# Kernel tuning notes

Measured on AMD Instinct MI355X. Metric: run time of the kernel, lower is better.

Reference implementation:

```python
import math
import jax, jax.numpy as jnp
import numpy as np

B, T, C, H = 4, 2048, 1024, 16
HS = C // H


def setup_inputs() -> dict:
    key = jax.random.key(0)
    ks = jax.random.split(key, 5)
    s_in = 1.0 / math.sqrt(C)
    return {
        "x": jax.random.normal(ks[0], (B, T, C), dtype=jnp.float32),
        "w_attn": jax.random.normal(ks[1], (C, 3 * C), dtype=jnp.float32) * s_in,
        "b_attn": jax.random.normal(ks[2], (3 * C,), dtype=jnp.float32) * 0.02,
        "w_proj": jax.random.normal(ks[3], (C, C), dtype=jnp.float32) * s_in,
        "b_proj": jax.random.normal(ks[4], (C,), dtype=jnp.float32) * 0.02,
    }


def reference(x, w_attn, b_attn, w_proj, b_proj):
    Bx, Tx, Cx = x.shape
    hs = Cx // H
    qkv = x @ w_attn + b_attn  # [B, T, 3C]
    q, k, v = jnp.split(qkv, 3, axis=-1)
    # [B, H, T, hs]
    q = q.reshape(Bx, Tx, H, hs).transpose(0, 2, 1, 3)
    k = k.reshape(Bx, Tx, H, hs).transpose(0, 2, 1, 3)
    v = v.reshape(Bx, Tx, H, hs).transpose(0, 2, 1, 3)
    scale = 1.0 / math.sqrt(hs)
    att = jnp.einsum("bhqd,bhkd->bhqk", q, k) * scale  # [B, H, T, T]
    causal = jnp.tril(jnp.ones((Tx, Tx), dtype=bool))
    att = jnp.where(causal, att, -jnp.inf)
    att = jax.nn.softmax(att, axis=-1)
    y = jnp.einsum("bhqk,bhkd->bhqd", att, v)  # [B, H, T, hs]
    y = y.transpose(0, 2, 1, 3).reshape(Bx, Tx, Cx)
    return y @ w_proj + b_proj
```

## Files before the change

kernel.cpp:

```cpp
#include <hip/hip_runtime.h>
#include <stdint.h>

#define Bn 4
#define Tn 2048
#define Cn 1024
#define Hn 16
#define HSn 64
#define Mn (Bn*Tn)
#define N1n (3*Cn)

typedef unsigned short u16;
typedef unsigned int u32;
typedef __attribute__((ext_vector_type(8))) short short8;
typedef __attribute__((ext_vector_type(4))) float f32x4;
typedef __attribute__((ext_vector_type(16))) float f32x16;

#define QSCf (0.125f * 1.44269504f)

__device__ __forceinline__ u16 f2bf(float f){
  u32 u = __float_as_uint(f);
  u += 0x7fffu + ((u >> 16) & 1u);
  return (u16)(u >> 16);
}

__device__ __forceinline__ u32 pkbf(float lo, float hi_){
  u32 r; asm("v_cvt_pk_bf16_f32 %0, %1, %2" : "=v"(r) : "v"(lo), "v"(hi_)); return r;
}

__device__ __forceinline__ float fexp2(float x){
  float r; asm("v_exp_f32 %0, %1" : "=v"(r) : "v"(x)); return r;
}

__device__ __forceinline__ float fmax3(float a, float b, float c){
  float r; asm("v_max3_f32 %0, %1, %2, %3" : "=v"(r) : "v"(a), "v"(b), "v"(c)); return r;
}

__device__ __forceinline__ void plswap(u32 &a, u32 &b){
  auto r = __builtin_amdgcn_permlane32_swap(a, b, false, false);
  a = r[0]; b = r[1];
}

__device__ __forceinline__ void gload_lds16(const void* g, void* l){
  __builtin_amdgcn_global_load_lds(
      (const __attribute__((address_space(1))) u32*)g,
      (__attribute__((address_space(3))) u32*)l, 16, 0, 0);
}

#define BARRIER() __builtin_amdgcn_s_barrier()
#define CFENCE() asm volatile("" ::: "memory")

__device__ __forceinline__ void tcvt_body(const float* __restrict__ in,
                                          u16* __restrict__ out,
                                          int R, int Cc, int bxx, int byy,
                                          float sh[64][68]){
  int tid = threadIdx.x;
  int c0 = bxx*64, r0 = byy*64;
  int rr = tid >> 4, c4 = (tid & 15) * 4;
  #pragma unroll
  for (int p=0;p<4;p++){
    int r = rr + 16*p;
    *(float4*)&sh[r][c4] = *(const float4*)&in[(size_t)(r0+r)*Cc + c0 + c4];
  }
  __syncthreads();
  #pragma unroll
  for (int p=0;p<4;p++){
    int oc = rr + 16*p;
    u32 w0 = (u32)f2bf(sh[c4+0][oc]) | ((u32)f2bf(sh[c4+1][oc]) << 16);
    u32 w1 = (u32)f2bf(sh[c4+2][oc]) | ((u32)f2bf(sh[c4+3][oc]) << 16);
    uint2 pk; pk.x = w0; pk.y = w1;
    *(uint2*)&out[(size_t)(c0+oc)*R + r0 + c4] = pk;
  }
}

__global__ __launch_bounds__(256)
void k_pre(const float* __restrict__ x, const float* __restrict__ wa,
           const float* __restrict__ wp, u16* __restrict__ xb,
           u16* __restrict__ waT, u16* __restrict__ wpT){
  __shared__ float sh[64][68];
  int bid = blockIdx.x;
  if (bid < 4096){
    int i = bid*256 + threadIdx.x;
    const float4* p = (const float4*)(x) + (size_t)i*2;
    float4 a = p[0], b = p[1];
    uint4 r;
    r.x = (u32)f2bf(a.x) | ((u32)f2bf(a.y) << 16);
    r.y = (u32)f2bf(a.z) | ((u32)f2bf(a.w) << 16);
    r.z = (u32)f2bf(b.x) | ((u32)f2bf(b.y) << 16);
    r.w = (u32)f2bf(b.z) | ((u32)f2bf(b.w) << 16);
    *((uint4*)(xb) + i) = r;
  } else if (bid < 4096 + 768){
    int b2 = bid - 4096;
    tcvt_body(wa, waT, Cn, N1n, b2 % 48, b2 / 48, sh);
  } else {
    int b3 = bid - 4864;
    tcvt_body(wp, wpT, Cn, Cn, b3 % 16, b3 / 16, sh);
  }
}

template <int MODE>
__global__ __launch_bounds__(256, 2)
void k_gemm2(const u16* __restrict__ A, const u16* __restrict__ Bt,
             const float* __restrict__ bias, void* __restrict__ Cout,
             u16* __restrict__ vt, int Nn_, int byPerXcd)
{
  extern __shared__ char smem[];
  const int nkt = 16;
  int tid = threadIdx.x;
  int wave = tid >> 6, lane = tid & 63, g = lane >> 4, cl = lane & 15;
  int wm = wave >> 1, wn = wave & 1;

  int xcd = blockIdx.x & 7, idx = blockIdx.x >> 3;
  int by = xcd * byPerXcd + (idx % byPerXcd);
  int bx = idx / byPerXcd;
  int m0 = by * 128, n0 = bx * 128;

  int srow = tid >> 3;
  int scolb = (tid & 7) << 4;
  int ssw = scolb ^ ((srow & 7) << 4);
  const char* Agp = (const char*)A  + (size_t)(m0 + srow) * 2048 + ssw;
  const char* Bgp = (const char*)Bt + (size_t)(n0 + srow) * 2048 + ssw;

  #define STG(t_, b_) { \
    const char* ag = Agp + (size_t)(t_)*128; \
    const char* bg = Bgp + (size_t)(t_)*128; \
    char* ab = smem + (b_)*32768 + (wave<<10); \
    char* bb = ab + 16384; \
    gload_lds16(ag,          ab); \
    gload_lds16(ag+ 65536,   ab+4096); \
    gload_lds16(ag+131072,   ab+8192); \
    gload_lds16(ag+196608,   ab+12288); \
    gload_lds16(bg,          bb); \
    gload_lds16(bg+ 65536,   bb+4096); \
    gload_lds16(bg+131072,   bb+8192); \
    gload_lds16(bg+196608,   bb+12288); }

  f32x4 acc[4][4];
  #pragma unroll
  for (int i=0;i<4;i++)
    #pragma unroll
    for (int j=0;j<4;j++) acc[i][j] = (f32x4){0.f,0.f,0.f,0.f};

  STG(0, 0);

  for (int t=0; t<nkt; ++t){
    int b = t & 1;
    if (t+1 < nkt){
      STG(t+1, b^1);
      asm volatile("s_waitcnt vmcnt(8)" ::: "memory");
    } else {
      asm volatile("s_waitcnt vmcnt(0)" ::: "memory");
    }
    BARRIER(); CFENCE();
    const char* Asb = smem + b*32768;
    const char* Bsb = Asb + 16384;
    short8 a[4][2], bq[4][2];
    #pragma unroll
    for (int i=0;i<4;i++){
      int row = wm*64 + i*16 + cl;
      #pragma unroll
      for (int ks=0;ks<2;ks++)
        a[i][ks] = *(const short8*)(Asb + row*128 + ((ks*64 + g*16) ^ ((row&7)<<4)));
    }
    #pragma unroll
    for (int j=0;j<4;j++){
      int row = wn*64 + j*16 + cl;
      #pragma unroll
      for (int ks=0;ks<2;ks++)
        bq[j][ks] = *(const short8*)(Bsb + row*128 + ((ks*64 + g*16) ^ ((row&7)<<4)));
    }
    __builtin_amdgcn_s_setprio(1);
    #pragma unroll
    for (int ks=0;ks<2;ks++)
      #pragma unroll
      for (int i=0;i<4;i++)
        #pragma unroll
        for (int j=0;j<4;j++)
          acc[i][j] = __builtin_amdgcn_mfma_f32_16x16x32_bf16(a[i][ks], bq[j][ks], acc[i][j], 0, 0, 0);
    __builtin_amdgcn_s_setprio(0);
    CFENCE(); BARRIER(); CFENCE();
  }
  #undef STG

  #pragma unroll
  for (int jj=0;jj<4;jj++){
    int col = n0 + wn*64 + jj*16 + cl;
    float bj = bias[col];
    if (MODE == 0){
      #pragma unroll
      for (int i=0;i<4;i++){
        int rowb = m0 + wm*64 + i*16 + g*4;
        #pragma unroll
        for (int r=0;r<4;r++)
          ((float*)Cout)[(size_t)(rowb+r)*Nn_ + col] = acc[i][jj][r] + bj;
      }
    } else if (col < 2*Cn){
      float sc = (col < Cn) ? QSCf : 1.0f;
      #pragma unroll
      for (int i=0;i<4;i++){
        int rowb = m0 + wm*64 + i*16 + g*4;
        #pragma unroll
        for (int r=0;r<4;r++)
          ((u16*)Cout)[(size_t)(rowb+r)*Nn_ + col] = f2bf((acc[i][jj][r] + bj) * sc);
      }
    } else {
      int hd = col - 2*Cn;
      #pragma unroll
      for (int i=0;i<4;i++){
        int rowb = m0 + wm*64 + i*16 + g*4;
        int bb = rowb >> 11, tt = rowb & 2047;
        u16* dst = vt + (((size_t)(bb*16 + (hd>>6)))*64 + (hd&63))*2048 + tt;
        uint2 pk;
        pk.x = (u32)f2bf(acc[i][jj][0]+bj) | ((u32)f2bf(acc[i][jj][1]+bj) << 16);
        pk.y = (u32)f2bf(acc[i][jj][2]+bj) | ((u32)f2bf(acc[i][jj][3]+bj) << 16);
        *(uint2*)dst = pk;
      }
    }
  }
}

__global__ __launch_bounds__(256, 4)
void k_attn(const u16* __restrict__ qkv, const u16* __restrict__ vt, u16* __restrict__ yb){
  __shared__ __align__(16) u16 Ks[2][64*64];
  __shared__ __align__(16) u16 Vs[2][64*64];
  int tid = threadIdx.x, wave = tid >> 6, lane = tid & 63;
  int ql = lane & 31, hi = lane >> 5;
  int blk = blockIdx.x;
  int xcd = blk & 7, rest = blk >> 3;
  int bh  = xcd + 8*(rest & 7);
  int qtsel = rest >> 3;
  int a_ = qtsel & 3, g_ = qtsel >> 2;
  int qt = (g_==0) ? (15 - a_) : (g_==1) ? (7 - a_) : (g_==2) ? (8 + a_) : a_;
  int b = bh >> 4, h = bh & 15;

  const u16* Kbase = qkv + (size_t)b*Tn*N1n + Cn + h*HSn;
  const u16* Vbase = vt  + (size_t)bh*HSn*Tn;

  auto STAGE = [&](int bufi, int kt){
    int kb_ = kt*64;
    #pragma unroll
    for (int it=0; it<2; ++it){
      int off = it*4096 + tid*16;
      int row = off >> 7;
      int cb  = off & 127;
      int gc  = (cb ^ ((row & 7) << 4)) >> 1;
      gload_lds16(Kbase + (size_t)(kb_ + row)*N1n + gc,
                  (char*)&Ks[bufi][0] + it*4096 + (wave << 10));
      gload_lds16(Vbase + (size_t)row*Tn + kb_ + gc,
                  (char*)&Vs[bufi][0] + it*4096 + (wave << 10));
    }
  };

  int q0 = qt * 128;
  int qw0 = q0 + wave*32;
  int qg  = qw0 + ql;
  int ntiles = 2*qt + 2;

  const u16* Qp = qkv + (size_t)(b*Tn + qg)*N1n + h*HSn;
  short8 qf[4];
  #pragma unroll
  for (int dc=0; dc<4; ++dc) qf[dc] = *(const short8*)&Qp[dc*16 + hi*8];

  short8 ones;
  #pragma unroll
  for (int r=0; r<8; ++r) ones[r] = (short)0x3F80;

  f32x16 accO[2], accL;
  #pragma unroll
  for (int f=0; f<2; ++f)
    #pragma unroll
    for (int r=0; r<16; ++r) accO[f][r] = 0.f;
  #pragma unroll
  for (int r=0; r<16; ++r) accL[r] = 0.f;
  float m_ = -1e30f;

  int xsw = (ql & 7) << 4;

  auto PVS = [&](const f32x16& sx, int pb, int voff, const char* Vsb){
    u32 w0 = pkbf(sx[pb+0], sx[pb+1]);
    u32 w1 = pkbf(sx[pb+2], sx[pb+3]);
    u32 w2 = pkbf(sx[pb+4], sx[pb+5]);
    u32 w3 = pkbf(sx[pb+6], sx[pb+7]);
    plswap(w0, w2);
    plswap(w1, w3);
    union { u32 w[4]; short8 v; } pu;
    pu.w[0] = w0; pu.w[1] = w1; pu.w[2] = w2; pu.w[3] = w3;
    __builtin_amdgcn_s_setprio(1);
    #pragma unroll
    for (int f=0; f<2; ++f){
      short8 vf = *(const short8*)(Vsb + ((f*32 + ql) << 7) + ((voff + hi*16) ^ xsw));
      accO[f] = __builtin_amdgcn_mfma_f32_32x32x16_bf16(vf, pu.v, accO[f], 0, 0, 0);
    }
    accL = __builtin_amdgcn_mfma_f32_32x32x16_bf16(ones, pu.v, accL, 0, 0, 0);
    __builtin_amdgcn_s_setprio(0);
  };

  STAGE(0, 0);
  int buf = 0;

  for (int kt=0; kt<ntiles; ++kt){
    if (kt+1 < ntiles){
      STAGE(buf^1, kt+1);
      asm volatile("s_waitcnt vmcnt(4)" ::: "memory");
    } else {
      asm volatile("s_waitcnt vmcnt(0)" ::: "memory");
    }
    BARRIER(); CFENCE();
    const char* Ksb = (const char*)&Ks[buf][0];
    const char* Vsb = (const char*)&Vs[buf][0];
    if (kt*64 + 63 <= qw0){
      f32x16 s0, s1;
      #pragma unroll
      for (int r=0; r<16; ++r){ s0[r]=0.f; s1[r]=0.f; }
      __builtin_amdgcn_s_setprio(1);
      #pragma unroll
      for (int dc=0; dc<4; ++dc){
        short8 kf0 = *(const short8*)(Ksb + ((     ql) << 7) + ((dc*32 + hi*16) ^ xsw));
        short8 kf1 = *(const short8*)(Ksb + ((32 + ql) << 7) + ((dc*32 + hi*16) ^ xsw));
        s0 = __builtin_amdgcn_mfma_f32_32x32x16_bf16(kf0, qf[dc], s0, 0, 0, 0);
        s1 = __builtin_amdgcn_mfma_f32_32x32x16_bf16(kf1, qf[dc], s1, 0, 0, 0);
      }
      __builtin_amdgcn_s_setprio(0);
      float a0 = fmax3(s0[0], s0[1], s0[2]);
      float a1 = fmax3(s0[3], s0[4], s0[5]);
      float a2 = fmax3(s0[6], s0[7], s0[8]);
      float a3 = fmax3(s0[9], s0[10], s0[11]);
      float a4 = fmax3(s0[12], s0[13], s0[14]);
      float ta = fmaxf(fmax3(a0, a1, a2), fmax3(a3, a4, s0[15]));
      float b0 = fmax3(s1[0], s1[1], s1[2]);
      float b1 = fmax3(s1[3], s1[4], s1[5]);
      float b2 = fmax3(s1[6], s1[7], s1[8]);
      float b3 = fmax3(s1[9], s1[10], s1[11]);
      float b4 = fmax3(s1[12], s1[13], s1[14]);
      float tb = fmaxf(fmax3(b0, b1, b2), fmax3(b3, b4, s1[15]));
      float tm = fmaxf(ta, tb);
      { u32 ua = __float_as_uint(tm), ub = ua; plswap(ua, ub);
        tm = fmaxf(__uint_as_float(ua), __uint_as_float(ub)); }
      if (!__all(tm - m_ <= 8.0f)){
        float mn = fmaxf(m_, tm);
        float al = fexp2(m_ - mn);
        m_ = mn;
        accL[0] *= al;
        #pragma unroll
        for (int f=0; f<2; ++f)
          #pragma unroll
          for (int r=0; r<16; ++r) accO[f][r] *= al;
      }
      #pragma unroll
      for (int r=0; r<16; ++r) s0[r] = fexp2(s0[r] - m_);
      PVS(s0, 0,  0, Vsb);
      PVS(s0, 8, 32, Vsb);
      #pragma unroll
      for (int r=0; r<16; ++r) s1[r] = fexp2(s1[r] - m_);
      PVS(s1, 0, 64, Vsb);
      PVS(s1, 8, 96, Vsb);
    } else {
      #pragma unroll
      for (int ksub=0; ksub<2; ++ksub){
        int kbase = kt*64 + ksub*32;
        if (kbase <= qw0 + 31){
          f32x16 s;
          #pragma unroll
          for (int r=0; r<16; ++r) s[r] = 0.f;
          __builtin_amdgcn_s_setprio(1);
          #pragma unroll
          for (int dc=0; dc<4; ++dc){
            short8 kf = *(const short8*)(Ksb + ((ksub*32 + ql) << 7)
                            + ((dc*32 + hi*16) ^ xsw));
            s = __builtin_amdgcn_mfma_f32_32x32x16_bf16(kf, qf[dc], s, 0, 0, 0);
          }
          __builtin_amdgcn_s_setprio(0);
          if (kbase + 31 > qw0){
            #pragma unroll
            for (int r=0; r<16; ++r){
              int krow = kbase + (r&3) + 8*(r>>2) + 4*hi;
              s[r] = (krow > qg) ? -1e30f : s[r];
            }
          }
          float r0 = fmax3(s[0], s[1], s[2]);
          float r1 = fmax3(s[3], s[4], s[5]);
          float r2 = fmax3(s[6], s[7], s[8]);
          float r3 = fmax3(s[9], s[10], s[11]);
          float r4 = fmax3(s[12], s[13], s[14]);
          float tm = fmaxf(fmax3(r0, r1, r2), fmax3(r3, r4, s[15]));
          { u32 ua = __float_as_uint(tm), ub = ua; plswap(ua, ub);
            tm = fmaxf(__uint_as_float(ua), __uint_as_float(ub)); }
          if (!__all(tm - m_ <= 8.0f)){
            float mn = fmaxf(m_, tm);
            float al = fexp2(m_ - mn);
            m_ = mn;
            accL[0] *= al;
            #pragma unroll
            for (int f=0; f<2; ++f)
              #pragma unroll
              for (int r=0; r<16; ++r) accO[f][r] *= al;
          }
          #pragma unroll
          for (int r=0; r<16; ++r) s[r] = fexp2(s[r] - m_);
          PVS(s, 0, ksub*64,      Vsb);
          PVS(s, 8, ksub*64 + 32, Vsb);
        }
      }
    }
    CFENCE(); BARRIER();
    buf ^= 1;
  }

  float rl = 1.0f / accL[0];
  u16* yp = yb + (size_t)(b*Tn + qg)*Cn + h*HSn;
  #pragma unroll
  for (int f=0; f<2; ++f)
    #pragma unroll
    for (int rq=0; rq<4; ++rq){
      int d0 = f*32 + rq*8 + hi*4;
      float v0 = accO[f][rq*4+0]*rl, v1 = accO[f][rq*4+1]*rl;
      float v2 = accO[f][rq*4+2]*rl, v3 = accO[f][rq*4+3]*rl;
      uint2 pk2;
      pk2.x = (u32)f2bf(v0) | ((u32)f2bf(v1) << 16);
      pk2.y = (u32)f2bf(v2) | ((u32)f2bf(v3) << 16);
      *(uint2*)&yp[d0] = pk2;
    }
}

extern "C" void kernel_launch(void* const* d_in, const int* in_sizes, int n_in,
                              void* d_out, int out_size, void* d_ws, size_t ws_size,
                              hipStream_t stream)
{
  const float* x      = (const float*)d_in[0];
  const float* w_attn = (const float*)d_in[1];
  const float* b_attn = (const float*)d_in[2];
  const float* w_proj = (const float*)d_in[3];
  const float* b_proj = (const float*)d_in[4];
  float* out = (float*)d_out;
  char* ws = (char*)d_ws;

  size_t off = 0;
  u16* xb  = (u16*)(ws + off); off += (size_t)Mn*Cn*2;
  u16* waT = (u16*)(ws + off); off += (size_t)N1n*Cn*2;
  u16* wpT = (u16*)(ws + off); off += (size_t)Cn*Cn*2;
  u16* qkv = (u16*)(ws + off); off += (size_t)Mn*N1n*2;
  u16* vt  = (u16*)(ws + off); off += (size_t)Bn*Hn*HSn*Tn*2;
  u16* yb  = (u16*)(ws + off); off += (size_t)Mn*Cn*2;

  (void)hipFuncSetAttribute((const void*)k_gemm2<1>,
        hipFuncAttributeMaxDynamicSharedMemorySize, 65536);
  (void)hipFuncSetAttribute((const void*)k_gemm2<0>,
        hipFuncAttributeMaxDynamicSharedMemorySize, 65536);

  k_pre<<<dim3(5120), 256, 0, stream>>>(x, w_attn, w_proj, xb, waT, wpT);
  k_gemm2<1><<<dim3((Mn/128)*(N1n/128)), 256, 65536, stream>>>(xb, waT, b_attn, qkv, vt, N1n, 8);
  k_attn<<<dim3(1024), 256, 0, stream>>>(qkv, vt, yb);
  k_gemm2<0><<<dim3((Mn/128)*(Cn/128)), 256, 65536, stream>>>(yb, wpT, b_proj, out, nullptr, Cn, 8);
}
```

Baseline: 143.2 us.

## Split long causal query tiles across two blocks and merge partials

```diff
diff --git a/kernel.cpp b/kernel.cpp
--- a/kernel.cpp
+++ b/kernel.cpp
@@ -219,7 +219,9 @@
 }
 
 __global__ __launch_bounds__(256, 4)
-void k_attn(const u16* __restrict__ qkv, const u16* __restrict__ vt, u16* __restrict__ yb){
+void k_attn(const u16* __restrict__ qkv, const u16* __restrict__ vt,
+            u16* __restrict__ yb, u16* __restrict__ Opart,
+            float* __restrict__ mpart, float* __restrict__ lpart){
   __shared__ __align__(16) u16 Ks[2][64*64];
   __shared__ __align__(16) u16 Vs[2][64*64];
   int tid = threadIdx.x, wave = tid >> 6, lane = tid & 63;
@@ -227,9 +229,12 @@
   int blk = blockIdx.x;
   int xcd = blk & 7, rest = blk >> 3;
   int bh  = xcd + 8*(rest & 7);
-  int qtsel = rest >> 3;
-  int a_ = qtsel & 3, g_ = qtsel >> 2;
-  int qt = (g_==0) ? (15 - a_) : (g_==1) ? (7 - a_) : (g_==2) ? (8 + a_) : a_;
+  int item = rest >> 3;
+  int grp = item/3, kind = item - grp*3;
+  int qt, lo, hi_t; bool partial = (kind != 2);
+  if (!partial){ qt = 7-grp; lo = 0; hi_t = 2*qt+2; }
+  else { qt = 15-grp; if (kind==0){ lo = 0; hi_t = qt+1; } else { lo = qt+1; hi_t = 2*qt+2; } }
+  int pslot = (bh*8 + (qt-8))*2 + kind;
   int b = bh >> 4, h = bh & 15;
 
   const u16* Kbase = qkv + (size_t)b*Tn*N1n + Cn + h*HSn;
@@ -253,7 +258,6 @@
   int q0 = qt * 128;
   int qw0 = q0 + wave*32;
   int qg  = qw0 + ql;
-  int ntiles = 2*qt + 2;
 
   const u16* Qp = qkv + (size_t)(b*Tn + qg)*N1n + h*HSn;
   short8 qf[4];
@@ -294,11 +298,11 @@
     __builtin_amdgcn_s_setprio(0);
   };
 
-  STAGE(0, 0);
+  STAGE(0, lo);
   int buf = 0;
 
-  for (int kt=0; kt<ntiles; ++kt){
-    if (kt+1 < ntiles){
+  for (int kt=lo; kt<hi_t; ++kt){
+    if (kt+1 < hi_t){
       STAGE(buf^1, kt+1);
       asm volatile("s_waitcnt vmcnt(4)" ::: "memory");
     } else {
@@ -405,20 +409,76 @@
     buf ^= 1;
   }
 
-  float rl = 1.0f / accL[0];
-  u16* yp = yb + (size_t)(b*Tn + qg)*Cn + h*HSn;
-  #pragma unroll
-  for (int f=0; f<2; ++f)
-    #pragma unroll
-    for (int rq=0; rq<4; ++rq){
-      int d0 = f*32 + rq*8 + hi*4;
-      float v0 = accO[f][rq*4+0]*rl, v1 = accO[f][rq*4+1]*rl;
-      float v2 = accO[f][rq*4+2]*rl, v3 = accO[f][rq*4+3]*rl;
-      uint2 pk2;
-      pk2.x = (u32)f2bf(v0) | ((u32)f2bf(v1) << 16);
-      pk2.y = (u32)f2bf(v2) | ((u32)f2bf(v3) << 16);
-      *(uint2*)&yp[d0] = pk2;
-    }
+  if (partial){
+    int qlocal = wave*32 + ql;
+    u16* op = Opart + ((size_t)pslot*128 + qlocal)*64;
+    #pragma unroll
+    for (int f=0; f<2; ++f)
+      #pragma unroll
+      for (int rq=0; rq<4; ++rq){
+        int d0 = f*32 + rq*8 + hi*4;
+        uint2 pk2;
+        pk2.x = (u32)f2bf(accO[f][rq*4+0]) | ((u32)f2bf(accO[f][rq*4+1]) << 16);
+        pk2.y = (u32)f2bf(accO[f][rq*4+2]) | ((u32)f2bf(accO[f][rq*4+3]) << 16);
+        *(uint2*)&op[d0] = pk2;
+      }
+    if (hi == 0){
+      mpart[pslot*128 + qlocal] = m_;
+      lpart[pslot*128 + qlocal] = accL[0];
+    }
+  } else {
+    float rl = 1.0f / accL[0];
+    u16* yp = yb + (size_t)(b*Tn + qg)*Cn + h*HSn;
+    #pragma unroll
+    for (int f=0; f<2; ++f)
+      #pragma unroll
+      for (int rq=0; rq<4; ++rq){
+        int d0 = f*32 + rq*8 + hi*4;
+        float v0 = accO[f][rq*4+0]*rl, v1 = accO[f][rq*4+1]*rl;
+        float v2 = accO[f][rq*4+2]*rl, v3 = accO[f][rq*4+3]*rl;
+        uint2 pk2;
+        pk2.x = (u32)f2bf(v0) | ((u32)f2bf(v1) << 16);
+        pk2.y = (u32)f2bf(v2) | ((u32)f2bf(v3) << 16);
+        *(uint2*)&yp[d0] = pk2;
+      }
+  }
+}
+
+__global__ __launch_bounds__(256)
+void k_merge(const u16* __restrict__ Op, const float* __restrict__ mp,
+             const float* __restrict__ lp, u16* __restrict__ yb){
+  int mslot = blockIdx.x;
+  int bh = mslot >> 3, qt = 8 + (mslot & 7);
+  int b = bh >> 4, h = bh & 15;
+  int t = threadIdx.x;
+  int q = t >> 1, dh = (t & 1) * 32;
+  int s0 = mslot*2, s1 = s0 + 1;
+  float m1 = mp[s0*128 + q], m2 = mp[s1*128 + q];
+  float l1 = lp[s0*128 + q], l2 = lp[s1*128 + q];
+  float mm = fmaxf(m1, m2);
+  float w1 = fexp2(m1 - mm), w2 = fexp2(m2 - mm);
+  float rl = 1.0f / (l1*w1 + l2*w2);
+  w1 *= rl; w2 *= rl;
+  const u16* p1 = Op + ((size_t)s0*128 + q)*64 + dh;
+  const u16* p2 = Op + ((size_t)s1*128 + q)*64 + dh;
+  u16* yp = yb + ((size_t)b*Tn + qt*128 + q)*Cn + h*HSn + dh;
+  #pragma unroll
+  for (int i=0; i<4; ++i){
+    uint4 A = *(const uint4*)(p1 + i*8);
+    uint4 C = *(const uint4*)(p2 + i*8);
+    const u32* aw = (const u32*)&A;
+    const u32* cw = (const u32*)&C;
+    uint4 R; u32* rw = (u32*)&R;
+    #pragma unroll
+    for (int j=0; j<4; ++j){
+      float alo = __uint_as_float(aw[j] << 16);
+      float ahi = __uint_as_float(aw[j] & 0xffff0000u);
+      float clo = __uint_as_float(cw[j] << 16);
+      float chi = __uint_as_float(cw[j] & 0xffff0000u);
+      rw[j] = pkbf(alo*w1 + clo*w2, ahi*w1 + chi*w2);
+    }
+    *(uint4*)(yp + i*8) = R;
+  }
 }
 
 extern "C" void kernel_launch(void* const* d_in, const int* in_sizes, int n_in,
@@ -441,6 +501,10 @@
   u16* vt  = (u16*)(ws + off); off += (size_t)Bn*Hn*HSn*Tn*2;
   u16* yb  = (u16*)(ws + off); off += (size_t)Mn*Cn*2;
 
+  u16*   Opart = xb;
+  float* mpart = (float*)waT;
+  float* lpart = (float*)waT + 1024*128;
+
   (void)hipFuncSetAttribute((const void*)k_gemm2<1>,
         hipFuncAttributeMaxDynamicSharedMemorySize, 65536);
   (void)hipFuncSetAttribute((const void*)k_gemm2<0>,
@@ -448,6 +512,7 @@
 
   k_pre<<<dim3(5120), 256, 0, stream>>>(x, w_attn, w_proj, xb, waT, wpT);
   k_gemm2<1><<<dim3((Mn/128)*(N1n/128)), 256, 65536, stream>>>(xb, waT, b_attn, qkv, vt, N1n, 8);
-  k_attn<<<dim3(1024), 256, 0, stream>>>(qkv, vt, yb);
+  k_attn<<<dim3(1536), 256, 0, stream>>>(qkv, vt, yb, Opart, mpart, lpart);
+  k_merge<<<dim3(512), 256, 0, stream>>>(Opart, mpart, lpart, yb);
   k_gemm2<0><<<dim3((Mn/128)*(Cn/128)), 256, 65536, stream>>>(yb, wpT, b_proj, out, nullptr, Cn, 8);
 }
```

Result: slower. 153.5 us (+7.2%).

## Use a 256x256-tile, 512-thread GEMM kernel for the QKV projection

Applied to the files above, without the earlier changes.

```diff
diff --git a/kernel.cpp b/kernel.cpp
--- a/kernel.cpp
+++ b/kernel.cpp
@@ -97,11 +97,126 @@
   }
 }
 
-template <int MODE>
+__global__ __launch_bounds__(512, 1)
+void k_gemm3(const u16* __restrict__ A, const u16* __restrict__ Bt,
+             const float* __restrict__ bias, u16* __restrict__ qkv,
+             u16* __restrict__ vt)
+{
+  extern __shared__ char smem[];
+  const int nkt = 16;
+  int tid = threadIdx.x;
+  int wave = tid >> 6, lane = tid & 63, g = lane >> 4, cl = lane & 15;
+  int wm = wave >> 1, wn = wave & 1;
+
+  int xcd = blockIdx.x & 7, idx = blockIdx.x >> 3;
+  int by = xcd*4 + (idx & 3);
+  int bx = idx >> 2;
+  int m0 = by * 256, n0 = bx * 256;
+
+  int srow = tid >> 3;
+  int scolb = (tid & 7) << 4;
+  int ssw = scolb ^ ((srow & 7) << 4);
+  const char* Agp = (const char*)A  + (size_t)(m0 + srow) * 2048 + ssw;
+  const char* Bgp = (const char*)Bt + (size_t)(n0 + srow) * 2048 + ssw;
+
+  #define STG(t_, b_) { \
+    const char* ag = Agp + (size_t)(t_)*128; \
+    const char* bg = Bgp + (size_t)(t_)*128; \
+    char* ab = smem + (b_)*65536 + (wave<<10); \
+    char* bb = ab + 32768; \
+    gload_lds16(ag,           ab); \
+    gload_lds16(ag + 131072,  ab +  8192); \
+    gload_lds16(ag + 262144,  ab + 16384); \
+    gload_lds16(ag + 393216,  ab + 24576); \
+    gload_lds16(bg,           bb); \
+    gload_lds16(bg + 131072,  bb +  8192); \
+    gload_lds16(bg + 262144,  bb + 16384); \
+    gload_lds16(bg + 393216,  bb + 24576); }
+
+  f32x4 acc[4][8];
+  #pragma unroll
+  for (int i=0;i<4;i++)
+    #pragma unroll
+    for (int j=0;j<8;j++) acc[i][j] = (f32x4){0.f,0.f,0.f,0.f};
+
+  STG(0, 0);
+
+  for (int t=0; t<nkt; ++t){
+    int b = t & 1;
+    if (t+1 < nkt){
+      STG(t+1, b^1);
+      asm volatile("s_waitcnt vmcnt(8)" ::: "memory");
+    } else {
+      asm volatile("s_waitcnt vmcnt(0)" ::: "memory");
+    }
+    BARRIER(); CFENCE();
+    const char* Asb = smem + b*65536;
+    const char* Bsb = Asb + 32768;
+    short8 a[4][2];
+    #pragma unroll
+    for (int i=0;i<4;i++){
+      int row = wm*64 + i*16 + cl;
+      #pragma unroll
+      for (int ks=0;ks<2;ks++)
+        a[i][ks] = *(const short8*)(Asb + row*128 + ((ks*64 + g*16) ^ ((row&7)<<4)));
+    }
+    #pragma unroll
+    for (int jh=0; jh<2; ++jh){
+      short8 bq[4][2];
+      #pragma unroll
+      for (int j4=0;j4<4;j4++){
+        int row = wn*128 + jh*64 + j4*16 + cl;
+        #pragma unroll
+        for (int ks=0;ks<2;ks++)
+          bq[j4][ks] = *(const short8*)(Bsb + row*128 + ((ks*64 + g*16) ^ ((row&7)<<4)));
+      }
+      __builtin_amdgcn_s_setprio(1);
+      #pragma unroll
+      for (int ks=0;ks<2;ks++)
+        #pragma unroll
+        for (int i=0;i<4;i++)
+          #pragma unroll
+          for (int j4=0;j4<4;j4++)
+            acc[i][jh*4+j4] = __builtin_amdgcn_mfma_f32_16x16x32_bf16(a[i][ks], bq[j4][ks], acc[i][jh*4+j4], 0, 0, 0);
+      __builtin_amdgcn_s_setprio(0);
+    }
+    CFENCE(); BARRIER(); CFENCE();
+  }
+  #undef STG
+
+  #pragma unroll
+  for (int jj=0;jj<8;jj++){
+    int col = n0 + wn*128 + jj*16 + cl;
+    float bj = bias[col];
+    if (col < 2*Cn){
+      float sc = (col < Cn) ? QSCf : 1.0f;
+      #pragma unroll
+      for (int i=0;i<4;i++){
+        int rowb = m0 + wm*64 + i*16 + g*4;
+        #pragma unroll
+        for (int r=0;r<4;r++)
+          qkv[(size_t)(rowb+r)*N1n + col] = f2bf((acc[i][jj][r] + bj) * sc);
+      }
+    } else {
+      int hd = col - 2*Cn;
+      #pragma unroll
+      for (int i=0;i<4;i++){
+        int rowb = m0 + wm*64 + i*16 + g*4;
+        int bb = rowb >> 11, tt = rowb & 2047;
+        u16* dst = vt + (((size_t)(bb*16 + (hd>>6)))*64 + (hd&63))*2048 + tt;
+        uint2 pk;
+        pk.x = (u32)f2bf(acc[i][jj][0]+bj) | ((u32)f2bf(acc[i][jj][1]+bj) << 16);
+        pk.y = (u32)f2bf(acc[i][jj][2]+bj) | ((u32)f2bf(acc[i][jj][3]+bj) << 16);
+        *(uint2*)dst = pk;
+      }
+    }
+  }
+}
+
 __global__ __launch_bounds__(256, 2)
 void k_gemm2(const u16* __restrict__ A, const u16* __restrict__ Bt,
-             const float* __restrict__ bias, void* __restrict__ Cout,
-             u16* __restrict__ vt, int Nn_, int byPerXcd)
+             const float* __restrict__ bias, float* __restrict__ Cout,
+             int Nn_, int byPerXcd)
 {
   extern __shared__ char smem[];
   const int nkt = 16;
@@ -185,35 +300,12 @@
   for (int jj=0;jj<4;jj++){
     int col = n0 + wn*64 + jj*16 + cl;
     float bj = bias[col];
-    if (MODE == 0){
-      #pragma unroll
-      for (int i=0;i<4;i++){
-        int rowb = m0 + wm*64 + i*16 + g*4;
-        #pragma unroll
-        for (int r=0;r<4;r++)
-          ((float*)Cout)[(size_t)(rowb+r)*Nn_ + col] = acc[i][jj][r] + bj;
-      }
-    } else if (col < 2*Cn){
-      float sc = (col < Cn) ? QSCf : 1.0f;
-      #pragma unroll
-      for (int i=0;i<4;i++){
-        int rowb = m0 + wm*64 + i*16 + g*4;
-        #pragma unroll
-        for (int r=0;r<4;r++)
-          ((u16*)Cout)[(size_t)(rowb+r)*Nn_ + col] = f2bf((acc[i][jj][r] + bj) * sc);
-      }
-    } else {
-      int hd = col - 2*Cn;
-      #pragma unroll
-      for (int i=0;i<4;i++){
-        int rowb = m0 + wm*64 + i*16 + g*4;
-        int bb = rowb >> 11, tt = rowb & 2047;
-        u16* dst = vt + (((size_t)(bb*16 + (hd>>6)))*64 + (hd&63))*2048 + tt;
-        uint2 pk;
-        pk.x = (u32)f2bf(acc[i][jj][0]+bj) | ((u32)f2bf(acc[i][jj][1]+bj) << 16);
-        pk.y = (u32)f2bf(acc[i][jj][2]+bj) | ((u32)f2bf(acc[i][jj][3]+bj) << 16);
-        *(uint2*)dst = pk;
-      }
+    #pragma unroll
+    for (int i=0;i<4;i++){
+      int rowb = m0 + wm*64 + i*16 + g*4;
+      #pragma unroll
+      for (int r=0;r<4;r++)
+        Cout[(size_t)(rowb+r)*Nn_ + col] = acc[i][jj][r] + bj;
     }
   }
 }
@@ -441,13 +533,13 @@
   u16* vt  = (u16*)(ws + off); off += (size_t)Bn*Hn*HSn*Tn*2;
   u16* yb  = (u16*)(ws + off); off += (size_t)Mn*Cn*2;
 
-  (void)hipFuncSetAttribute((const void*)k_gemm2<1>,
+  (void)hipFuncSetAttribute((const void*)k_gemm3,
+        hipFuncAttributeMaxDynamicSharedMemorySize, 131072);
+  (void)hipFuncSetAttribute((const void*)k_gemm2,
         hipFuncAttributeMaxDynamicSharedMemorySize, 65536);
-  (void)hipFuncSetAttribute((const void*)k_gemm2<0>,
-        hipFuncAttributeMaxDynamicSharedMemorySize, 65536);
 
   k_pre<<<dim3(5120), 256, 0, stream>>>(x, w_attn, w_proj, xb, waT, wpT);
-  k_gemm2<1><<<dim3((Mn/128)*(N1n/128)), 256, 65536, stream>>>(xb, waT, b_attn, qkv, vt, N1n, 8);
+  k_gemm3<<<dim3((Mn/256)*(N1n/256)), 512, 131072, stream>>>(xb, waT, b_attn, qkv, vt);
   k_attn<<<dim3(1024), 256, 0, stream>>>(qkv, vt, yb);
-  k_gemm2<0><<<dim3((Mn/128)*(Cn/128)), 256, 65536, stream>>>(yb, wpT, b_proj, out, nullptr, Cn, 8);
-}
+  k_gemm2<<<dim3((Mn/128)*(Cn/128)), 256, 65536, stream>>>(yb, wpT, b_proj, out, Cn, 8);
+}
```

Measured after the change: 160.9 us. 12.3% more time.
